# Kernel optimization log

Hardware: AMD Instinct MI355X
Metric: run time of the kernel (lower is better)

The kernel has to match this reference:

```python
import jax, jax.numpy as jnp
import numpy as np

B, C, F, H = 512, 80, 768, 256
EPS = 1e-5
THR = 0.5
SCALE = 1.0 / np.sqrt(H)


def _ln(z, g, b):
    m = jnp.mean(z, axis=-1, keepdims=True)
    v = jnp.mean((z - m) ** 2, axis=-1, keepdims=True)
    return (z - m) * jax.lax.rsqrt(v + EPS) * g + b


def setup_inputs() -> dict:
    key = jax.random.key(0)
    ks = jax.random.split(key, 12)
    w = 0.05  # weight scale for numerical sanity
    return {
        "x": jax.random.normal(ks[0], (B, C, H), jnp.float32),
        "visual_features": jax.random.normal(ks[1], (B, F), jnp.float32),
        "labels": jax.random.randint(ks[2], (B, C), 0, 2, jnp.int32),
        # visual_proj: Linear(F,H) + LayerNorm(H)
        "Wp": jax.random.normal(ks[3], (F, H), jnp.float32) * w,
        "bp": jnp.zeros((H,), jnp.float32),
        "gp": jnp.ones((H,), jnp.float32),
        "bep": jnp.zeros((H,), jnp.float32),
        # per-class extractors: stacked Linear(H,H) + LayerNorm(H)
        "Wc": jax.random.normal(ks[4], (C, H, H), jnp.float32) * w,
        "bc": jnp.zeros((C, H), jnp.float32),
        "gc": jnp.ones((C, H), jnp.float32),
        "bec": jnp.zeros((C, H), jnp.float32),
        # attention projections
        "Wq": jax.random.normal(ks[5], (H, H), jnp.float32) * w,
        "bq": jnp.zeros((H,), jnp.float32),
        "Wk": jax.random.normal(ks[6], (H, H), jnp.float32) * w,
        "bk": jnp.zeros((H,), jnp.float32),
        "Wv": jax.random.normal(ks[7], (H, H), jnp.float32) * w,
        "bv": jnp.zeros((H,), jnp.float32),
        "Wo": jax.random.normal(ks[8], (H, H), jnp.float32) * w,
        "bo": jnp.zeros((H,), jnp.float32),
    }


def reference(x, visual_features, labels, Wp, bp, gp, bep, Wc, bc, gc, bec,
              Wq, bq, Wk, bk, Wv, bv, Wo, bo):
    # visual_proj: Linear + LN + ReLU  -> (B,H)
    vis = jax.nn.relu(_ln(visual_features @ Wp + bp, gp, bep))
    # per-class extractor ensemble fused into one batched GEMM -> (B,C,H)
    z = jnp.einsum('bh,chk->bck', vis, Wc) + bc
    class_feats = jax.nn.relu(_ln(z, gc, bec))
    x = x + class_feats
    q = x @ Wq + bq
    k = x @ Wk + bk
    v = x @ Wv + bv
    scores = jnp.einsum('bch,bdh->bcd', q, k) * SCALE  # (B,C,C)
    scores = scores * (scores > THR).astype(scores.dtype)  # hard similarity mask
    label_mask = labels.astype(scores.dtype)[:, None, :] * 0.8 + 0.2
    scores = scores * label_mask
    attn = jax.nn.softmax(scores, axis=-1)
    out = jnp.einsum('bcd,bdh->bch', attn, v)
    return out @ Wo + bo
```

## Files before the change

### kernel.cpp

```cpp
#include <hip/hip_runtime.h>
#include <hip/hip_bf16.h>
#include <math.h>

#define Bq 512
#define Cq 80
#define Fq 768
#define Hq 256

constexpr float EPS   = 1e-5f;
constexpr float THR   = 0.5f;
constexpr float SCALE = 0.0625f;

using f32x4 = __attribute__((ext_vector_type(4))) float;
using s16x8 = __attribute__((ext_vector_type(8))) short;
using s16x4 = __attribute__((ext_vector_type(4))) short;

#define MFMA16 __builtin_amdgcn_mfma_f32_16x16x32_bf16


__device__ __forceinline__ float waveReduceSum(float v) {
#pragma unroll
  for (int m = 32; m >= 1; m >>= 1) v += __shfl_xor(v, m);
  return v;
}

__device__ __forceinline__ float bfu(unsigned short v) {
  return __uint_as_float(((unsigned)v) << 16);
}

__device__ __forceinline__ unsigned short f2bf(float f) {
  __hip_bfloat16 h = __float2bfloat16(f);
  return *reinterpret_cast<unsigned short*>(&h);
}

__device__ __forceinline__ int packOff(int tile, int kk8, int g, int l15, int e) {
  return ((tile * 8 + kk8) * 4 + g) * 128 + l15 * 8 + e;
}

__global__ __launch_bounds__(256) void k_visproj(
    const float* __restrict__ vf, const float* __restrict__ Wp,
    const float* __restrict__ bp, const float* __restrict__ gp,
    const float* __restrict__ bep,
    unsigned short* __restrict__ visPh, unsigned short* __restrict__ visPl) {
  __shared__ float vfs[Fq];
  __shared__ float red[4];
  const int b = blockIdx.x, h = threadIdx.x;
  for (int i = h; i < Fq; i += 256) vfs[i] = vf[b * Fq + i];
  __syncthreads();

  float acc = bp[h];
  for (int f = 0; f < Fq; f++) acc = fmaf(vfs[f], Wp[f * Hq + h], acc);

  const int w = h >> 6, lane = h & 63;
  float s = waveReduceSum(acc);
  if (lane == 0) red[w] = s;
  __syncthreads();
  const float mean = (red[0] + red[1] + red[2] + red[3]) * (1.0f / Hq);
  __syncthreads();
  const float d = acc - mean;
  s = waveReduceSum(d * d);
  if (lane == 0) red[w] = s;
  __syncthreads();
  const float var = (red[0] + red[1] + red[2] + red[3]) * (1.0f / Hq);
  float y = d * rsqrtf(var + EPS) * gp[h] + bep[h];
  y = fmaxf(y, 0.0f);
  const unsigned short hb = f2bf(y);
  const int off = packOff(b >> 4, h >> 5, (h & 31) >> 3, b & 15, h & 7);
  visPh[off] = hb;
  visPl[off] = f2bf(y - bfu(hb));
}

__global__ __launch_bounds__(256) void k_matmulM(
    const float* __restrict__ Wq, const float* __restrict__ Wk,
    const float* __restrict__ bq, const float* __restrict__ bk,
    unsigned short* __restrict__ MTph, unsigned short* __restrict__ MTpl,
    float* __restrict__ w1, float* __restrict__ w2, float* __restrict__ cqk) {
  const int i = blockIdx.x, j = threadIdx.x;
  const int wv = j >> 6, lane = j & 63;
  __shared__ float rowq[Hq];
  __shared__ float redA[4], redB[4], redC[4];
  rowq[j] = Wq[i * Hq + j];
  __syncthreads();
  float acc = 0.f;
  const float* wkr = Wk + (size_t)j * Hq;
  for (int h = 0; h < Hq; h += 4) {
    const float4 a = *reinterpret_cast<const float4*>(&rowq[h]);
    const float4 bb = *reinterpret_cast<const float4*>(&wkr[h]);
    acc = fmaf(a.x, bb.x, fmaf(a.y, bb.y, fmaf(a.z, bb.z, fmaf(a.w, bb.w, acc))));
  }
  const unsigned short hb = f2bf(acc);
  const int off = packOff(j >> 4, i >> 5, (i & 31) >> 3, j & 15, i & 7);
  MTph[off] = hb;
  MTpl[off] = f2bf(acc - bfu(hb));

  float p1 = rowq[j] * bk[j];
  float p2 = Wk[(size_t)i * Hq + j] * bq[j];
  float p3 = bq[j] * bk[j];
  p1 = waveReduceSum(p1);
  p2 = waveReduceSum(p2);
  p3 = waveReduceSum(p3);
  if (lane == 0) { redA[wv] = p1; redB[wv] = p2; redC[wv] = p3; }
  __syncthreads();
  if (j == 0) {
    w1[i] = redA[0] + redA[1] + redA[2] + redA[3];
    w2[i] = redB[0] + redB[1] + redB[2] + redB[3];
    if (i == 0) *cqk = redC[0] + redC[1] + redC[2] + redC[3];
  }
}

__global__ void k_prep(const float* __restrict__ Wc, const float* __restrict__ Wv,
                       const float* __restrict__ Wo,
                       unsigned short* __restrict__ WcTph, unsigned short* __restrict__ WcTpl,
                       unsigned short* __restrict__ WvTp, unsigned short* __restrict__ WoTp) {
  const int NWc = Cq * 32 * 256;
  const int NTOT = NWc + 2 * 32 * 256;
  for (int idx = blockIdx.x * blockDim.x + threadIdx.x; idx < NTOT;
       idx += gridDim.x * blockDim.x) {
    if (idx < NWc) {
      const int c = idx >> 13, k8 = (idx >> 8) & 31, n = idx & 255;
      const float* src = Wc + (size_t)c * 65536 + (size_t)k8 * 8 * 256 + n;
      s16x8 hh, ll;
#pragma unroll
      for (int e = 0; e < 8; e++) {
        const float v = src[e * 256];
        const unsigned short hb = f2bf(v);
        hh[e] = (short)hb;
        ll[e] = (short)f2bf(v - bfu(hb));
      }
      const int off = c * 65536 + packOff(n >> 4, k8 >> 2, k8 & 3, n & 15, 0);
      *reinterpret_cast<s16x8*>(WcTph + off) = hh;
      *reinterpret_cast<s16x8*>(WcTpl + off) = ll;
    } else {
      const int r = idx - NWc;
      const int which = r >> 13;
      const int r2 = r & 8191;
      const int k8 = r2 >> 8, n = r2 & 255;
      const float* src = (which == 0 ? Wv : Wo) + (size_t)k8 * 8 * 256 + n;
      s16x8 hh;
#pragma unroll
      for (int e = 0; e < 8; e++) hh[e] = (short)f2bf(src[e * 256]);
      const int off = packOff(n >> 4, k8 >> 2, k8 & 3, n & 15, 0);
      *reinterpret_cast<s16x8*>((which == 0 ? WvTp : WoTp) + off) = hh;
    }
  }
}

__global__ __launch_bounds__(256) void k_gemm1f(
    const unsigned short* __restrict__ visPh, const unsigned short* __restrict__ visPl,
    const unsigned short* __restrict__ WcTph, const unsigned short* __restrict__ WcTpl,
    const float* __restrict__ x, const float* __restrict__ bc,
    const float* __restrict__ gc, const float* __restrict__ bec,
    const float* __restrict__ w1, const float* __restrict__ w2,
    unsigned short* __restrict__ Xgh, unsigned short* __restrict__ Xgl,
    float* __restrict__ u, float* __restrict__ vv) {
  const int blk = blockIdx.x;
  const int mapped = (blk & 7) * 160 + (blk >> 3);
  const int c = mapped >> 4;
  const int bx = mapped & 15;
  const int b0 = bx * 32;
  const int tid = threadIdx.x;
  const int wvi = tid >> 6, lane = tid & 63;
  const int l15 = lane & 15, l4 = lane >> 4;

  __shared__ float Zs[32][268];

  f32x4 acc[2][4];
#pragma unroll
  for (int m = 0; m < 2; m++)
#pragma unroll
    for (int n = 0; n < 4; n++) acc[m][n] = (f32x4){0.f, 0.f, 0.f, 0.f};

  const unsigned short* Bh = WcTph + (size_t)c * 65536;
  const unsigned short* Bl = WcTpl + (size_t)c * 65536;

  for (int kk8 = 0; kk8 < 8; kk8++) {
    s16x8 ah[2], al[2], bh[4], bl[4];
#pragma unroll
    for (int m = 0; m < 2; m++) {
      const int off = packOff(bx * 2 + m, kk8, l4, l15, 0);
      ah[m] = *reinterpret_cast<const s16x8*>(visPh + off);
      al[m] = *reinterpret_cast<const s16x8*>(visPl + off);
    }
#pragma unroll
    for (int n = 0; n < 4; n++) {
      const int off = packOff(wvi * 4 + n, kk8, l4, l15, 0);
      bh[n] = *reinterpret_cast<const s16x8*>(Bh + off);
      bl[n] = *reinterpret_cast<const s16x8*>(Bl + off);
    }
#pragma unroll
    for (int m = 0; m < 2; m++)
#pragma unroll
      for (int n = 0; n < 4; n++) {
        acc[m][n] = MFMA16(ah[m], bh[n], acc[m][n], 0, 0, 0);
        acc[m][n] = MFMA16(ah[m], bl[n], acc[m][n], 0, 0, 0);
        acc[m][n] = MFMA16(al[m], bh[n], acc[m][n], 0, 0, 0);
      }
  }

#pragma unroll
  for (int m = 0; m < 2; m++)
#pragma unroll
    for (int n = 0; n < 4; n++) {
      const int col = wvi * 64 + n * 16 + l15;
      const float bcv = bc[c * Hq + col];
#pragma unroll
      for (int r = 0; r < 4; r++)
        Zs[m * 16 + l4 * 4 + r][col] = acc[m][n][r] + bcv;
    }
  __syncthreads();

  const int row = tid >> 3, sub = tid & 7;
  const int grow = b0 + row;
  const size_t xrow = ((size_t)grow * Cq + c) * Hq;
  float zz[32];
  float sum = 0.f, sumsq = 0.f;
#pragma unroll
  for (int kq = 0; kq < 8; kq++) {
    const float4 z = *reinterpret_cast<const float4*>(&Zs[row][sub * 4 + kq * 32]);
    zz[4 * kq + 0] = z.x; zz[4 * kq + 1] = z.y;
    zz[4 * kq + 2] = z.z; zz[4 * kq + 3] = z.w;
    sum += z.x + z.y + z.z + z.w;
    sumsq += z.x * z.x + z.y * z.y + z.z * z.z + z.w * z.w;
  }
#pragma unroll
  for (int msk = 4; msk >= 1; msk >>= 1) {
    sum += __shfl_xor(sum, msk);
    sumsq += __shfl_xor(sumsq, msk);
  }
  const float mean = sum * (1.0f / Hq);
  const float var = sumsq * (1.0f / Hq) - mean * mean;
  const float inv = rsqrtf(var + EPS);

  float pu = 0.f, pv = 0.f;
#pragma unroll
  for (int kq = 0; kq < 8; kq++) {
    const int col = sub * 4 + kq * 32;
    const float4 xv = *reinterpret_cast<const float4*>(&x[xrow + col]);
    const float xr[4] = {xv.x, xv.y, xv.z, xv.w};
    s16x4 hh, ll;
#pragma unroll
    for (int e = 0; e < 4; e++) {
      float tt = (zz[4 * kq + e] - mean) * inv * gc[c * Hq + col + e] + bec[c * Hq + col + e];
      tt = fmaxf(tt, 0.f);
      const float xp = xr[e] + tt;
      const unsigned short hb2 = f2bf(xp);
      hh[e] = (short)hb2;
      ll[e] = (short)f2bf(xp - bfu(hb2));
      pu = fmaf(xp, w1[col + e], pu);
      pv = fmaf(xp, w2[col + e], pv);
    }
    *reinterpret_cast<s16x4*>(Xgh + xrow + col) = hh;
    *reinterpret_cast<s16x4*>(Xgl + xrow + col) = ll;
  }
#pragma unroll
  for (int msk = 4; msk >= 1; msk >>= 1) {
    pu += __shfl_xor(pu, msk);
    pv += __shfl_xor(pv, msk);
  }
  if (sub == 0) {
    u[(size_t)grow * Cq + c] = pu;
    vv[(size_t)grow * Cq + c] = pv;
  }
}

__global__ __launch_bounds__(256) void k_gemm2p(
    unsigned short* Xh, unsigned short* Xl,
    const unsigned short* __restrict__ MTph, const unsigned short* __restrict__ MTpl,
    const unsigned short* __restrict__ WvTp, const float* __restrict__ bv,
    unsigned short* __restrict__ XMh, unsigned short* __restrict__ XMl,
    unsigned short* __restrict__ Vt) {
  __shared__ __attribute__((aligned(16))) unsigned short Xsh[32 * 264];
  __shared__ __attribute__((aligned(16))) unsigned short Xsl[32 * 264];
  __shared__ __attribute__((aligned(16))) unsigned short XMsh[8192];
  __shared__ __attribute__((aligned(16))) unsigned short XMsl[8192];
  __shared__ __attribute__((aligned(16))) unsigned short Vst[256 * 24];

  const int blk = blockIdx.x;
  const int r0 = blk * 32;
  const int tid = threadIdx.x;
  const int wvi = tid >> 6, lane = tid & 63;
  const int l15 = lane & 15, l4 = lane >> 4;

#pragma unroll
  for (int it = 0; it < 4; it++) {
    const int ch = it * 256 + tid;
    const int rr = ch >> 5, cc = ch & 31;
    const size_t gsrc = (size_t)(r0 + rr) * Hq + cc * 8;
    *reinterpret_cast<s16x8*>(&Xsh[rr * 264 + cc * 8]) =
        *reinterpret_cast<const s16x8*>(Xh + gsrc);
    *reinterpret_cast<s16x8*>(&Xsl[rr * 264 + cc * 8]) =
        *reinterpret_cast<const s16x8*>(Xl + gsrc);
  }
  __syncthreads();

  f32x4 acc[2][4];
#pragma unroll
  for (int m = 0; m < 2; m++)
#pragma unroll
    for (int n = 0; n < 4; n++) acc[m][n] = (f32x4){0.f, 0.f, 0.f, 0.f};

  for (int kk8 = 0; kk8 < 8; kk8++) {
    s16x8 ah[2], al[2], bh[4], bl[4];
#pragma unroll
    for (int m = 0; m < 2; m++) {
      const int lo = (m * 16 + l15) * 264 + kk8 * 32 + l4 * 8;
      ah[m] = *reinterpret_cast<const s16x8*>(&Xsh[lo]);
      al[m] = *reinterpret_cast<const s16x8*>(&Xsl[lo]);
    }
#pragma unroll
    for (int n = 0; n < 4; n++) {
      const int off = packOff(wvi * 4 + n, kk8, l4, l15, 0);
      bh[n] = *reinterpret_cast<const s16x8*>(MTph + off);
      bl[n] = *reinterpret_cast<const s16x8*>(MTpl + off);
    }
#pragma unroll
    for (int m = 0; m < 2; m++)
#pragma unroll
      for (int n = 0; n < 4; n++) {
        acc[m][n] = MFMA16(ah[m], bh[n], acc[m][n], 0, 0, 0);
        acc[m][n] = MFMA16(ah[m], bl[n], acc[m][n], 0, 0, 0);
        acc[m][n] = MFMA16(al[m], bh[n], acc[m][n], 0, 0, 0);
      }
  }

#pragma unroll
  for (int m = 0; m < 2; m++)
#pragma unroll
    for (int n = 0; n < 4; n++) {
      const int col = wvi * 64 + n * 16 + l15;
      const int kk8c = col >> 5, gc = (col & 31) >> 3, ec = col & 7;
#pragma unroll
      for (int r = 0; r < 4; r++) {
        const int off = ((m * 8 + kk8c) * 4 + gc) * 128 + (l4 * 4 + r) * 8 + ec;
        const float v = acc[m][n][r];
        const unsigned short hb = f2bf(v);
        XMsh[off] = hb;
        XMsl[off] = f2bf(v - bfu(hb));
      }
    }
  __syncthreads();

#pragma unroll
  for (int it = 0; it < 4; it++) {
    const int ch = it * 256 + tid;
    const size_t gdst = (size_t)blk * 8192 + ch * 8;
    *reinterpret_cast<s16x8*>(XMh + gdst) = *reinterpret_cast<const s16x8*>(&XMsh[ch * 8]);
    *reinterpret_cast<s16x8*>(XMl + gdst) = *reinterpret_cast<const s16x8*>(&XMsl[ch * 8]);
    const int l15c = ch & 15, g3 = (ch >> 4) & 3, kk = (ch >> 6) & 7, mm = ch >> 9;
    const int lsrc = (mm * 16 + l15c) * 264 + kk * 32 + g3 * 8;
    *reinterpret_cast<s16x8*>(Xh + gdst) = *reinterpret_cast<const s16x8*>(&Xsh[lsrc]);
    *reinterpret_cast<s16x8*>(Xl + gdst) = *reinterpret_cast<const s16x8*>(&Xsl[lsrc]);
  }

  for (int m = 0; m < 2; m++) {
    f32x4 vac[4];
#pragma unroll
    for (int n = 0; n < 4; n++) vac[n] = (f32x4){0.f, 0.f, 0.f, 0.f};
    for (int kk8 = 0; kk8 < 8; kk8++) {
      const int lo = (m * 16 + l15) * 264 + kk8 * 32 + l4 * 8;
      const s16x8 ah = *reinterpret_cast<const s16x8*>(&Xsh[lo]);
      const s16x8 al = *reinterpret_cast<const s16x8*>(&Xsl[lo]);
#pragma unroll
      for (int n = 0; n < 4; n++) {
        const s16x8 bh = *reinterpret_cast<const s16x8*>(
            WvTp + packOff(wvi * 4 + n, kk8, l4, l15, 0));
        vac[n] = MFMA16(ah, bh, vac[n], 0, 0, 0);
        vac[n] = MFMA16(al, bh, vac[n], 0, 0, 0);
      }
    }
#pragma unroll
    for (int n = 0; n < 4; n++) {
      const int col = (wvi * 4 + n) * 16 + l15;
      const float bvv = bv[col];
#pragma unroll
      for (int r = 0; r < 4; r++)
        Vst[col * 24 + l4 * 4 + r] = f2bf(vac[n][r] + bvv);
    }
    __syncthreads();
    {
      const int gt = blk * 2 + m;
      const int bb = gt / 5, ct = gt - bb * 5;
      const unsigned short* src = &Vst[tid * 24];
      const s16x8 va = *reinterpret_cast<const s16x8*>(src);
      const s16x8 vb2 = *reinterpret_cast<const s16x8*>(src + 8);
      const size_t ga = ((size_t)bb * Hq + tid) * Cq + ct * 16;
      *reinterpret_cast<s16x8*>(Vt + ga) = va;
      *reinterpret_cast<s16x8*>(Vt + ga + 8) = vb2;
    }
    __syncthreads();
  }
}

__global__ __launch_bounds__(320) void k_attn5(
    const unsigned short* __restrict__ XPh, const unsigned short* __restrict__ XPl,
    const unsigned short* __restrict__ XMh, const unsigned short* __restrict__ XMl,
    const unsigned short* __restrict__ Vt, const int* __restrict__ labels,
    const float* __restrict__ u, const float* __restrict__ vv,
    const float* __restrict__ cqk, const unsigned short* __restrict__ WoTp,
    const float* __restrict__ bo, float* __restrict__ out) {
  __shared__ unsigned short Pl_[80][104];
  __shared__ unsigned short Olds[80][264];
  __shared__ float us[80], vvs[80], lms[80];

  const int b = blockIdx.x, t = threadIdx.x;
  const int w = t >> 6, lane = t & 63;
  const int l15 = lane & 15, g = lane >> 4;

  if (t < 80) {
    us[t] = u[b * Cq + t];
    vvs[t] = vv[b * Cq + t];
    lms[t] = (float)labels[b * Cq + t] * 0.8f + 0.2f;
  }

  f32x4 sacc[5];
#pragma unroll
  for (int mt = 0; mt < 5; mt++) sacc[mt] = (f32x4){0.f, 0.f, 0.f, 0.f};

  for (int kk8 = 0; kk8 < 8; kk8++) {
    const int offB = packOff(b * 5 + w, kk8, g, l15, 0);
    const s16x8 bh = *reinterpret_cast<const s16x8*>(XMh + offB);
    const s16x8 bl = *reinterpret_cast<const s16x8*>(XMl + offB);
#pragma unroll
    for (int mt = 0; mt < 5; mt++) {
      const int offA = packOff(b * 5 + mt, kk8, g, l15, 0);
      const s16x8 ah = *reinterpret_cast<const s16x8*>(XPh + offA);
      const s16x8 al = *reinterpret_cast<const s16x8*>(XPl + offA);
      sacc[mt] = MFMA16(ah, bh, sacc[mt], 0, 0, 0);
      sacc[mt] = MFMA16(ah, bl, sacc[mt], 0, 0, 0);
      sacc[mt] = MFMA16(al, bh, sacc[mt], 0, 0, 0);
    }
  }
  __syncthreads();

  const int i = 16 * w + l15;
  const float ui = us[i];
  const float cq = *cqk;
  float p[5][4];
  float mx = -1e30f;
#pragma unroll
  for (int mt = 0; mt < 5; mt++)
#pragma unroll
    for (int r = 0; r < 4; r++) {
      const int j = 16 * mt + 4 * g + r;
      float sc = (sacc[mt][r] + ui + vvs[j] + cq) * SCALE;
      sc = (sc > THR) ? sc : 0.0f;
      sc *= lms[j];
      p[mt][r] = sc;
      mx = fmaxf(mx, sc);
    }
  mx = fmaxf(mx, __shfl_xor(mx, 16));
  mx = fmaxf(mx, __shfl_xor(mx, 32));
  float sum = 0.f;
#pragma unroll
  for (int mt = 0; mt < 5; mt++)
#pragma unroll
    for (int r = 0; r < 4; r++) {
      const float e = __expf(p[mt][r] - mx);
      p[mt][r] = e;
      sum += e;
    }
  sum += __shfl_xor(sum, 16);
  sum += __shfl_xor(sum, 32);
  const float inv = 1.0f / sum;

#pragma unroll
  for (int mt = 0; mt < 5; mt++) {
    uint2 pk;
    pk.x = (unsigned)f2bf(p[mt][0] * inv) | ((unsigned)f2bf(p[mt][1] * inv) << 16);
    pk.y = (unsigned)f2bf(p[mt][2] * inv) | ((unsigned)f2bf(p[mt][3] * inv) << 16);
    *reinterpret_cast<uint2*>(reinterpret_cast<char*>(&Pl_[i][0]) + 32 * mt + 8 * g) = pk;
  }
  if (t < 160) {
    const uint4 z = {0u, 0u, 0u, 0u};
    *reinterpret_cast<uint4*>(reinterpret_cast<char*>(&Pl_[t >> 1][0]) + 160 + 16 * (t & 1)) = z;
  }
  __syncthreads();

  s16x8 pa[3];
#pragma unroll
  for (int ks = 0; ks < 3; ks++)
    pa[ks] = *reinterpret_cast<const s16x8*>(
        reinterpret_cast<const char*>(&Pl_[i][0]) + 64 * ks + 16 * g);

  f32x4 oacc[16];
#pragma unroll
  for (int n = 0; n < 16; n++) oacc[n] = (f32x4){0.f, 0.f, 0.f, 0.f};

  const size_t vbase = (size_t)b * Hq * Cq;
#pragma unroll 4
  for (int n = 0; n < 16; n++) {
    const size_t hrow = vbase + (size_t)(16 * n + l15) * Cq + 8 * g;
#pragma unroll
    for (int ks = 0; ks < 3; ks++) {
      const s16x8 vb = *reinterpret_cast<const s16x8*>(Vt + hrow + 32 * ks);
      oacc[n] = MFMA16(pa[ks], vb, oacc[n], 0, 0, 0);
    }
  }

#pragma unroll
  for (int n = 0; n < 16; n++)
#pragma unroll
    for (int r = 0; r < 4; r++)
      Olds[16 * w + 4 * g + r][16 * n + l15] = f2bf(oacc[n][r]);

  f32x4 acc2[16];
#pragma unroll
  for (int n = 0; n < 16; n++) acc2[n] = (f32x4){0.f, 0.f, 0.f, 0.f};

  for (int ks = 0; ks < 8; ks++) {
    const s16x8 af = *reinterpret_cast<const s16x8*>(
        reinterpret_cast<const char*>(&Olds[16 * w + l15][0]) + 64 * ks + 16 * g);
#pragma unroll
    for (int n = 0; n < 16; n++) {
      const s16x8 bf = *reinterpret_cast<const s16x8*>(WoTp + packOff(n, ks, g, l15, 0));
      acc2[n] = MFMA16(af, bf, acc2[n], 0, 0, 0);
    }
  }

#pragma unroll
  for (int n = 0; n < 16; n++) {
    const float bov = bo[16 * n + l15];
#pragma unroll
    for (int r = 0; r < 4; r++)
      out[((size_t)b * Cq + 16 * w + 4 * g + r) * Hq + 16 * n + l15] =
          acc2[n][r] + bov;
  }
}

extern "C" void kernel_launch(void* const* d_in, const int* in_sizes, int n_in,
                              void* d_out, int out_size, void* d_ws, size_t ws_size,
                              hipStream_t stream) {
  const float* x   = (const float*)d_in[0];
  const float* vf  = (const float*)d_in[1];
  const int*   lab = (const int*)d_in[2];
  const float* Wp  = (const float*)d_in[3];
  const float* bp  = (const float*)d_in[4];
  const float* gp  = (const float*)d_in[5];
  const float* bep = (const float*)d_in[6];
  const float* Wc  = (const float*)d_in[7];
  const float* bc  = (const float*)d_in[8];
  const float* gc  = (const float*)d_in[9];
  const float* bec = (const float*)d_in[10];
  const float* Wq  = (const float*)d_in[11];
  const float* bq_ = (const float*)d_in[12];
  const float* Wk  = (const float*)d_in[13];
  const float* bk_ = (const float*)d_in[14];
  const float* Wv  = (const float*)d_in[15];
  const float* bv_ = (const float*)d_in[16];
  const float* Wo  = (const float*)d_in[17];
  const float* bo_ = (const float*)d_in[18];
  float* out = (float*)d_out;
  (void)ws_size; (void)in_sizes; (void)n_in; (void)out_size;

  char* W = (char*)d_ws;
  unsigned short* Xh    = (unsigned short*)(W + 0);
  unsigned short* Xl    = (unsigned short*)(W + 20971520);
  unsigned short* WcTph = (unsigned short*)(W + 41943040);
  unsigned short* WcTpl = (unsigned short*)(W + 52428800);
  unsigned short* XMh   = (unsigned short*)(W + 41943040);
  unsigned short* XMl   = (unsigned short*)(W + 62914560);
  unsigned short* Vt    = (unsigned short*)(W + 83886080);
  unsigned short* visPh = (unsigned short*)(W + 104857600);
  unsigned short* visPl = (unsigned short*)(W + 105119744);
  unsigned short* MTph  = (unsigned short*)(W + 105381888);
  unsigned short* MTpl  = (unsigned short*)(W + 105512960);
  unsigned short* WvTp  = (unsigned short*)(W + 105644032);
  unsigned short* WoTp  = (unsigned short*)(W + 105775104);
  float* w1  = (float*)(W + 105906176);
  float* w2  = (float*)(W + 105907200);
  float* cqk = (float*)(W + 105908224);
  float* u   = (float*)(W + 105908480);
  float* vvv = (float*)(W + 106072320);

  k_visproj<<<Bq, 256, 0, stream>>>(vf, Wp, bp, gp, bep, visPh, visPl);
  k_matmulM<<<Hq, 256, 0, stream>>>(Wq, Wk, bq_, bk_, MTph, MTpl, w1, w2, cqk);
  k_prep<<<1024, 256, 0, stream>>>(Wc, Wv, Wo, WcTph, WcTpl, WvTp, WoTp);
  k_gemm1f<<<1280, 256, 0, stream>>>(visPh, visPl, WcTph, WcTpl, x, bc, gc, bec,
                                     w1, w2, Xh, Xl, u, vvv);
  k_gemm2p<<<1280, 256, 0, stream>>>(Xh, Xl, MTph, MTpl, WvTp, bv_,
                                     XMh, XMl, Vt);
  k_attn5<<<Bq, 320, 0, stream>>>(Xh, Xl, XMh, XMl, Vt, lab, u, vvv, cqk,
                                  WoTp, bo_, out);
}
```

Baseline: 201.2 us.

## Stage global stores through LDS for coalesced writes and retile V layout

The gemm1 epilogue now writes the bf16 hi/lo X tiles into shared memory (reusing the Z buffer) and then copies them out with coalesced 16-byte stores. The V-transpose output in gemm2 becomes a contiguous per-tile [ct][h][16] layout written with linear vector stores, and the attention kernel's PV loads are changed to match, skipping the zero-padded class columns. The attention output epilogue stages fp32 results through the Olds shared buffer in two halves so each wave writes full float4 rows. These changes aim to cut uncoalesced global writes, at the cost of extra barriers and shared-memory traffic.

```diff
diff --git a/kernel.cpp b/kernel.cpp
--- a/kernel.cpp
+++ b/kernel.cpp
@@ -162,7 +162,9 @@
   const int wvi = tid >> 6, lane = tid & 63;
   const int l15 = lane & 15, l4 = lane >> 4;
 
-  __shared__ float Zs[32][268];
+  __shared__ __attribute__((aligned(16))) float Zs[32][268];
+  unsigned short* const Sh = reinterpret_cast<unsigned short*>(&Zs[0][0]);
+  unsigned short* const Sl = Sh + 32 * 264;
 
   f32x4 acc[2][4];
 #pragma unroll
@@ -230,6 +232,7 @@
   const float mean = sum * (1.0f / Hq);
   const float var = sumsq * (1.0f / Hq) - mean * mean;
   const float inv = rsqrtf(var + EPS);
+  __syncthreads();
 
   float pu = 0.f, pv = 0.f;
 #pragma unroll
@@ -249,8 +252,8 @@
       pu = fmaf(xp, w1[col + e], pu);
       pv = fmaf(xp, w2[col + e], pv);
     }
-    *reinterpret_cast<s16x4*>(Xgh + xrow + col) = hh;
-    *reinterpret_cast<s16x4*>(Xgl + xrow + col) = ll;
+    *reinterpret_cast<s16x4*>(&Sh[row * 264 + col]) = hh;
+    *reinterpret_cast<s16x4*>(&Sl[row * 264 + col]) = ll;
   }
 #pragma unroll
   for (int msk = 4; msk >= 1; msk >>= 1) {
@@ -260,6 +263,16 @@
   if (sub == 0) {
     u[(size_t)grow * Cq + c] = pu;
     vv[(size_t)grow * Cq + c] = pv;
+  }
+  __syncthreads();
+
+#pragma unroll
+  for (int it = 0; it < 4; it++) {
+    const int ch = it * 256 + tid;
+    const int rr = ch >> 5, cc = ch & 31;
+    const size_t gdst = ((size_t)(b0 + rr) * Cq + c) * Hq + cc * 8;
+    *reinterpret_cast<s16x8*>(Xgh + gdst) = *reinterpret_cast<const s16x8*>(&Sh[rr * 264 + cc * 8]);
+    *reinterpret_cast<s16x8*>(Xgl + gdst) = *reinterpret_cast<const s16x8*>(&Sl[rr * 264 + cc * 8]);
   }
 }
 
@@ -273,7 +286,7 @@
   __shared__ __attribute__((aligned(16))) unsigned short Xsl[32 * 264];
   __shared__ __attribute__((aligned(16))) unsigned short XMsh[8192];
   __shared__ __attribute__((aligned(16))) unsigned short XMsl[8192];
-  __shared__ __attribute__((aligned(16))) unsigned short Vst[256 * 24];
+  __shared__ __attribute__((aligned(16))) unsigned short Vst[256 * 16];
 
   const int blk = blockIdx.x;
   const int r0 = blk * 32;
@@ -372,20 +385,20 @@
     for (int n = 0; n < 4; n++) {
       const int col = (wvi * 4 + n) * 16 + l15;
       const float bvv = bv[col];
-#pragma unroll
-      for (int r = 0; r < 4; r++)
-        Vst[col * 24 + l4 * 4 + r] = f2bf(vac[n][r] + bvv);
+      s16x4 pk;
+#pragma unroll
+      for (int r = 0; r < 4; r++) pk[r] = (short)f2bf(vac[n][r] + bvv);
+      *reinterpret_cast<s16x4*>(&Vst[col * 16 + l4 * 4]) = pk;
     }
     __syncthreads();
     {
       const int gt = blk * 2 + m;
-      const int bb = gt / 5, ct = gt - bb * 5;
-      const unsigned short* src = &Vst[tid * 24];
-      const s16x8 va = *reinterpret_cast<const s16x8*>(src);
-      const s16x8 vb2 = *reinterpret_cast<const s16x8*>(src + 8);
-      const size_t ga = ((size_t)bb * Hq + tid) * Cq + ct * 16;
-      *reinterpret_cast<s16x8*>(Vt + ga) = va;
-      *reinterpret_cast<s16x8*>(Vt + ga + 8) = vb2;
+#pragma unroll
+      for (int it = 0; it < 2; it++) {
+        const int ch = it * 256 + tid;
+        *reinterpret_cast<s16x8*>(Vt + (size_t)gt * 4096 + ch * 8) =
+            *reinterpret_cast<const s16x8*>(&Vst[ch * 8]);
+      }
     }
     __syncthreads();
   }
@@ -398,8 +411,8 @@
     const float* __restrict__ u, const float* __restrict__ vv,
     const float* __restrict__ cqk, const unsigned short* __restrict__ WoTp,
     const float* __restrict__ bo, float* __restrict__ out) {
-  __shared__ unsigned short Pl_[80][104];
-  __shared__ unsigned short Olds[80][264];
+  __shared__ __attribute__((aligned(16))) unsigned short Pl_[80][104];
+  __shared__ __attribute__((aligned(16))) unsigned short Olds[80][264];
   __shared__ float us[80], vvs[80], lms[80];
 
   const int b = blockIdx.x, t = threadIdx.x;
@@ -486,13 +499,18 @@
 #pragma unroll
   for (int n = 0; n < 16; n++) oacc[n] = (f32x4){0.f, 0.f, 0.f, 0.f};
 
-  const size_t vbase = (size_t)b * Hq * Cq;
-#pragma unroll 4
+  const size_t vtb = (size_t)b * 5 * 4096;
+#pragma unroll
   for (int n = 0; n < 16; n++) {
-    const size_t hrow = vbase + (size_t)(16 * n + l15) * Cq + 8 * g;
 #pragma unroll
     for (int ks = 0; ks < 3; ks++) {
-      const s16x8 vb = *reinterpret_cast<const s16x8*>(Vt + hrow + 32 * ks);
+      const int c0 = 32 * ks + 8 * g;
+      s16x8 vb = (s16x8){0, 0, 0, 0, 0, 0, 0, 0};
+      if (c0 < 80) {
+        const int ct = c0 >> 4, off = c0 & 15;
+        vb = *reinterpret_cast<const s16x8*>(
+            Vt + vtb + (size_t)(ct * 256 + 16 * n + l15) * 16 + off);
+      }
       oacc[n] = MFMA16(pa[ks], vb, oacc[n], 0, 0, 0);
     }
   }
@@ -518,12 +536,28 @@
   }
 
 #pragma unroll
-  for (int n = 0; n < 16; n++) {
-    const float bov = bo[16 * n + l15];
-#pragma unroll
-    for (int r = 0; r < 4; r++)
-      out[((size_t)b * Cq + 16 * w + 4 * g + r) * Hq + 16 * n + l15] =
-          acc2[n][r] + bov;
+  for (int p2 = 0; p2 < 2; p2++) {
+    __syncthreads();
+    if ((g >> 1) == p2) {
+      float* Of = reinterpret_cast<float*>(&Olds[16 * w][0]);
+#pragma unroll
+      for (int n = 0; n < 16; n++) {
+        const float bov = bo[16 * n + l15];
+#pragma unroll
+        for (int r = 0; r < 4; r++)
+          Of[(4 * (g & 1) + r) * 256 + 16 * n + l15] = acc2[n][r] + bov;
+      }
+    }
+    __syncthreads();
+    {
+      const float* Of = reinterpret_cast<const float*>(&Olds[16 * w][0]);
+      float* orow = out + ((size_t)b * Cq + 16 * w + 8 * p2) * Hq;
+#pragma unroll
+      for (int j = 0; j < 8; j++) {
+        const float4 v4 = *reinterpret_cast<const float4*>(&Of[j * 256 + lane * 4]);
+        *reinterpret_cast<float4*>(&orow[(size_t)j * Hq + lane * 4]) = v4;
+      }
+    }
   }
 }
 
```

New measurement: 205.5 us. 2.1% more time.
